# Kernel optimization log

Measured on AMD Instinct MI355X. Metric: run time of the kernel, lower is better.

Reference implementation:

```python
import jax, jax.numpy as jnp
import numpy as np

D_MODEL, N_HEADS, D_FF = 1024, 16, 4096
B, L, PREFIX = 2, 2048, 512
EPS = 1e-5


def _ln(x, w, b):
    mu = jnp.mean(x, axis=-1, keepdims=True)
    var = jnp.mean((x - mu) ** 2, axis=-1, keepdims=True)
    return (x - mu) * jax.lax.rsqrt(var + EPS) * w + b


def setup_inputs() -> dict:
    key = jax.random.key(0)
    ks = jax.random.split(key, 5)
    d, f = D_MODEL, D_FF
    return {
        "x": jax.random.normal(ks[0], (B, L, d), jnp.float32),
        "ln1_w": jnp.ones((d,), jnp.float32),
        "ln1_b": jnp.zeros((d,), jnp.float32),
        "in_proj_w": jax.random.normal(ks[1], (3 * d, d), jnp.float32) / np.sqrt(d),
        "in_proj_b": jnp.zeros((3 * d,), jnp.float32),
        "out_w": jax.random.normal(ks[2], (d, d), jnp.float32) / np.sqrt(d),
        "out_b": jnp.zeros((d,), jnp.float32),
        "ln2_w": jnp.ones((d,), jnp.float32),
        "ln2_b": jnp.zeros((d,), jnp.float32),
        "fc1_w": jax.random.normal(ks[3], (f, d), jnp.float32) / np.sqrt(d),
        "fc1_b": jnp.zeros((f,), jnp.float32),
        "fc2_w": jax.random.normal(ks[4], (d, f), jnp.float32) / np.sqrt(f),
        "fc2_b": jnp.zeros((d,), jnp.float32),
        "prefix_len": PREFIX,
    }


def reference(x, ln1_w, ln1_b, in_proj_w, in_proj_b, out_w, out_b,
              ln2_w, ln2_b, fc1_w, fc1_b, fc2_w, fc2_b, prefix_len):
    Bv, Lv, d = x.shape
    H = N_HEADS
    hd = d // H
    m = prefix_len

    # additive prefix-decoder mask (L, L): allowed if j < m, or (i >= m and j <= i)
    i = jnp.arange(Lv)[:, None]
    j = jnp.arange(Lv)[None, :]
    allowed = (j < m) | ((i >= m) & (j <= i))
    mask = jnp.where(allowed, 0.0, -jnp.inf).astype(x.dtype)

    h = _ln(x, ln1_w, ln1_b)
    qkv = h @ in_proj_w.T + in_proj_b                      # [B, L, 3d]
    q, k, v = jnp.split(qkv, 3, axis=-1)
    q = q.reshape(Bv, Lv, H, hd)
    k = k.reshape(Bv, Lv, H, hd)
    v = v.reshape(Bv, Lv, H, hd)
    scale = 1.0 / np.sqrt(hd)
    scores = jnp.einsum("bihd,bjhd->bhij", q, k) * scale   # [B, H, L, L]
    attn = jax.nn.softmax(scores + mask, axis=-1)
    ctx = jnp.einsum("bhij,bjhd->bihd", attn, v).reshape(Bv, Lv, d)
    sa = ctx @ out_w.T + out_b
    x = x + sa

    h = _ln(x, ln2_w, ln2_b)
    ff = jax.nn.gelu(h @ fc1_w.T + fc1_b, approximate=False) @ fc2_w.T + fc2_b
    return x + ff
```

## Files before the change

kernel.cpp:

```cpp
#include <hip/hip_runtime.h>
#include <cstdint>
#include <cstddef>

#define DM   1024
#define NH   16
#define HD   64
#define DFF  4096
#define BB   2
#define LL   2048
#define MM   (BB*LL)

using short8 = __attribute__((ext_vector_type(8))) short;
using f32x4  = __attribute__((ext_vector_type(4))) float;

__device__ __forceinline__ unsigned short f2bf(float f) {
  union { float f; uint32_t u; } v; v.f = f;
  uint32_t u = v.u;
  uint32_t r = (u + 0x7fffu + ((u >> 16) & 1u)) >> 16;
  return (unsigned short)r;
}

__device__ __forceinline__ uint32_t cvtpk_bf16(float a, float b) {
  uint32_t r;
  asm("v_cvt_pk_bf16_f32 %0, %1, %2" : "=v"(r) : "v"(a), "v"(b));
  return r;
}

__device__ __forceinline__ float exp2_fast(float x) {
  float r;
  asm("v_exp_f32 %0, %1" : "=v"(r) : "v"(x));
  return r;
}

__device__ __forceinline__ float rcp_fast(float x) {
  float r;
  asm("v_rcp_f32 %0, %1" : "=v"(r) : "v"(x));
  return r;
}

__device__ __forceinline__ float gelu_tanh(float v) {
  float y = v * (0.7978845608028654f + 0.035677408136300125f * v * v);
  float e = exp2_fast(y * 2.885390081777927f);
  float tnh = 1.0f - 2.0f * rcp_fast(1.0f + e);
  return 0.5f * v * (1.0f + tnh);
}

#define GLDS16(gp, lp) \
  __builtin_amdgcn_global_load_lds((const __attribute__((address_space(1))) uint32_t*)(gp), \
                                   (__attribute__((address_space(3))) uint32_t*)(lp), 16, 0, 0)

__global__ __launch_bounds__(256) void convert_f32_bf16(const float* __restrict__ in,
                                                        unsigned short* __restrict__ out, int n4) {
  int i = blockIdx.x * 256 + threadIdx.x;
  if (i < n4) {
    float4 v = ((const float4*)in)[i];
    ushort4 o;
    o.x = f2bf(v.x); o.y = f2bf(v.y); o.z = f2bf(v.z); o.w = f2bf(v.w);
    ((ushort4*)out)[i] = o;
  }
}

__global__ __launch_bounds__(256) void convert4(const float* __restrict__ s0, unsigned short* __restrict__ d0, int n0,
                                                const float* __restrict__ s1, unsigned short* __restrict__ d1, int n1,
                                                const float* __restrict__ s2, unsigned short* __restrict__ d2, int n2,
                                                const float* __restrict__ s3, unsigned short* __restrict__ d3, int n3) {
  const int tid = blockIdx.x * 256 + threadIdx.x;
  const int stride = gridDim.x * 256;
  for (int i = tid; i < n0; i += stride) {
    float4 v = ((const float4*)s0)[i];
    ushort4 o; o.x = f2bf(v.x); o.y = f2bf(v.y); o.z = f2bf(v.z); o.w = f2bf(v.w);
    ((ushort4*)d0)[i] = o;
  }
  for (int i = tid; i < n1; i += stride) {
    float4 v = ((const float4*)s1)[i];
    ushort4 o; o.x = f2bf(v.x); o.y = f2bf(v.y); o.z = f2bf(v.z); o.w = f2bf(v.w);
    ((ushort4*)d1)[i] = o;
  }
  for (int i = tid; i < n2; i += stride) {
    float4 v = ((const float4*)s2)[i];
    ushort4 o; o.x = f2bf(v.x); o.y = f2bf(v.y); o.z = f2bf(v.z); o.w = f2bf(v.w);
    ((ushort4*)d2)[i] = o;
  }
  for (int i = tid; i < n3; i += stride) {
    float4 v = ((const float4*)s3)[i];
    ushort4 o; o.x = f2bf(v.x); o.y = f2bf(v.y); o.z = f2bf(v.z); o.w = f2bf(v.w);
    ((ushort4*)d3)[i] = o;
  }
}

__global__ __launch_bounds__(256) void ln_kernel(const float* __restrict__ x,
                                                 const float* __restrict__ w,
                                                 const float* __restrict__ b,
                                                 unsigned short* __restrict__ out) {
  int row = blockIdx.x, t = threadIdx.x;
  float4 v = ((const float4*)(x + (size_t)row * DM))[t];
  float s  = v.x + v.y + v.z + v.w;
  float sq = v.x*v.x + v.y*v.y + v.z*v.z + v.w*v.w;
  #pragma unroll
  for (int o = 32; o; o >>= 1) { s += __shfl_down(s, o); sq += __shfl_down(sq, o); }
  __shared__ float sh[8];
  if ((t & 63) == 0) { sh[t >> 6] = s; sh[4 + (t >> 6)] = sq; }
  __syncthreads();
  float S  = sh[0] + sh[1] + sh[2] + sh[3];
  float SQ = sh[4] + sh[5] + sh[6] + sh[7];
  float mu  = S * (1.0f / DM);
  float var = SQ * (1.0f / DM) - mu * mu;
  float rs  = rsqrtf(var + 1e-5f);
  float4 wv = ((const float4*)w)[t];
  float4 bv = ((const float4*)b)[t];
  ushort4 o;
  o.x = f2bf((v.x - mu) * rs * wv.x + bv.x);
  o.y = f2bf((v.y - mu) * rs * wv.y + bv.y);
  o.z = f2bf((v.z - mu) * rs * wv.z + bv.z);
  o.w = f2bf((v.w - mu) * rs * wv.w + bv.w);
  ((ushort4*)(out + (size_t)row * DM))[t] = o;
}

template <int EPI>
__global__ __launch_bounds__(512) void gemm8(const unsigned short* __restrict__ A,
                                             const unsigned short* __restrict__ Bw,
                                             const float* __restrict__ bias,
                                             unsigned short* __restrict__ Cout,
                                             int M, int N, int K, int lda, int ldb) {
  __shared__ unsigned short As[2][256 * 64];
  __shared__ unsigned short Bs[2][256 * 64];
  const int t = threadIdx.x;
  const int l = t & 63, lr = l & 15, lg = l >> 4;
  const int wid = t >> 6, wm = wid >> 2, wn = wid & 3;

  int bx = blockIdx.x, by = blockIdx.y;
  {
    const int gx = gridDim.x;
    const int total = gx * gridDim.y;
    if ((total & 7) == 0) {
      int lin = by * gx + bx;
      int lin2 = (lin & 7) * (total >> 3) + (lin >> 3);
      bx = lin2 % gx;
      by = lin2 / gx;
    }
  }
  const int m0 = by * 256, n0 = bx * 256;

  f32x4 acc[8][4];
  #pragma unroll
  for (int mi = 0; mi < 8; ++mi)
    #pragma unroll
    for (int ni = 0; ni < 4; ++ni) acc[mi][ni] = {0.f, 0.f, 0.f, 0.f};

  const int rowt = t >> 3, sw = (t & 7) ^ (rowt & 7);
  const unsigned short* Ag = A  + (size_t)(m0 + rowt) * lda + sw * 8;
  const unsigned short* Bg = Bw + (size_t)(n0 + rowt) * ldb + sw * 8;
  const size_t r64A = (size_t)64 * lda;
  const size_t r64B = (size_t)64 * ldb;

  const int rs = lr & 7;
  const int segA = (lg ^ rs) * 8;
  const int segB = ((lg + 4) ^ rs) * 8;

  const int nt = K >> 6;

  auto stage = [&](int kt, int buf) {
    const int k0 = kt << 6;
    char* Ad = (char*)&As[buf][0] + t * 16;
    char* Bd = (char*)&Bs[buf][0] + t * 16;
    #pragma unroll
    for (int g = 0; g < 4; ++g) GLDS16(Ag + k0 + g * r64A, Ad + g * 8192);
    #pragma unroll
    for (int g = 0; g < 4; ++g) GLDS16(Bg + k0 + g * r64B, Bd + g * 8192);
  };

  auto compute = [&](const unsigned short* __restrict__ Ab,
                     const unsigned short* __restrict__ Bb) {
    short8 bfr[4][2];
    #pragma unroll
    for (int ni = 0; ni < 4; ++ni) {
      const int row = wn * 64 + ni * 16 + lr;
      bfr[ni][0] = *(const short8*)&Bb[row * 64 + segA];
      bfr[ni][1] = *(const short8*)&Bb[row * 64 + segB];
    }
    __builtin_amdgcn_s_setprio(1);
    #pragma unroll
    for (int mp = 0; mp < 4; ++mp) {
      short8 af[2][2];
      #pragma unroll
      for (int q = 0; q < 2; ++q) {
        const int row = wm * 128 + (mp * 2 + q) * 16 + lr;
        af[q][0] = *(const short8*)&Ab[row * 64 + segA];
        af[q][1] = *(const short8*)&Ab[row * 64 + segB];
      }
      #pragma unroll
      for (int q = 0; q < 2; ++q)
        #pragma unroll
        for (int ni = 0; ni < 4; ++ni) {
          acc[mp * 2 + q][ni] = __builtin_amdgcn_mfma_f32_16x16x32_bf16(af[q][0], bfr[ni][0], acc[mp * 2 + q][ni], 0, 0, 0);
          acc[mp * 2 + q][ni] = __builtin_amdgcn_mfma_f32_16x16x32_bf16(af[q][1], bfr[ni][1], acc[mp * 2 + q][ni], 0, 0, 0);
        }
    }
    __builtin_amdgcn_s_setprio(0);
  };

  stage(0, 0);
  __syncthreads();

  for (int kt = 0; kt < nt; kt += 2) {
    if (kt + 1 < nt) stage(kt + 1, 1);
    compute(As[0], Bs[0]);
    __syncthreads();
    if (kt + 2 < nt) stage(kt + 2, 0);
    compute(As[1], Bs[1]);
    __syncthreads();
  }

  #pragma unroll
  for (int mi = 0; mi < 8; ++mi) {
    int row = m0 + wm * 128 + mi * 16 + lg * 4;
    #pragma unroll
    for (int ni = 0; ni < 4; ++ni) {
      int col = n0 + wn * 64 + ni * 16 + lr;
      float bv = bias[col];
      #pragma unroll
      for (int r = 0; r < 4; ++r) {
        float v = acc[mi][ni][r] + bv;
        size_t idx = (size_t)(row + r) * N + col;
        if (EPI == 0) {
          Cout[idx] = f2bf(v);
        } else {
          Cout[idx] = f2bf(gelu_tanh(v));
        }
      }
    }
  }
}

template <int EPI, int BM>
__global__ __launch_bounds__(256) void gemm_bt(const unsigned short* __restrict__ A,
                                               const unsigned short* __restrict__ Bw,
                                               const float* __restrict__ bias,
                                               const float* __restrict__ res,
                                               void* __restrict__ Cout,
                                               int M, int N, int K, int lda, int ldb) {
  constexpr int MI   = BM / 32;
  constexpr int ABUF = BM * 64;
  __shared__ unsigned short As[2 * ABUF];
  __shared__ unsigned short Bs[2 * 64 * 64];
  const int t = threadIdx.x;
  const int l = t & 63, lr = l & 15, lg = l >> 4;
  const int w = t >> 6, wm = w >> 1, wn = w & 1;

  int bx = blockIdx.x, by = blockIdx.y;
  {
    const int gx = gridDim.x;
    const int total = gx * gridDim.y;
    if ((total & 7) == 0) {
      int lin = by * gx + bx;
      int lin2 = (lin & 7) * (total >> 3) + (lin >> 3);
      bx = lin2 % gx;
      by = lin2 / gx;
    }
  }
  const int m0 = by * BM, n0 = bx * 64;

  f32x4 acc[MI][2];
  #pragma unroll
  for (int mi = 0; mi < MI; ++mi)
    #pragma unroll
    for (int ni = 0; ni < 2; ++ni) acc[mi][ni] = {0.f, 0.f, 0.f, 0.f};

  const int rowt = t >> 3, sw = (t & 7) ^ (rowt & 7);
  const unsigned short* Ag = A  + (size_t)(m0 + rowt) * lda + sw * 8;
  const unsigned short* Bg = Bw + (size_t)(n0 + rowt) * ldb + sw * 8;
  char* AsB = (char*)As + t * 16;
  char* BsB = (char*)Bs + t * 16;
  const size_t r32A = (size_t)32 * lda;
  const size_t r32B = (size_t)32 * ldb;

  const int rs = lr & 7;
  const int segA = (lg ^ rs) * 8;
  const int segB = ((lg + 4) ^ rs) * 8;

  #pragma unroll
  for (int g = 0; g < MI; ++g) GLDS16(Ag + g * r32A, AsB + g * 4096);
  GLDS16(Bg,        BsB);
  GLDS16(Bg + r32B, BsB + 4096);

  int cur = 0;
  for (int k0 = 0; k0 < K; k0 += 64, cur ^= 1) {
    __syncthreads();
    const int kn = k0 + 64;
    if (kn < K) {
      char* An = AsB + (cur ^ 1) * (ABUF * 2);
      char* Bn = BsB + (cur ^ 1) * 8192;
      #pragma unroll
      for (int g = 0; g < MI; ++g) GLDS16(Ag + kn + g * r32A, An + g * 4096);
      GLDS16(Bg + kn,        Bn);
      GLDS16(Bg + kn + r32B, Bn + 4096);
    }
    const unsigned short* Ab = As + cur * ABUF;
    const unsigned short* Bb = Bs + cur * (64 * 64);
    short8 af[MI][2], bfr[2][2];
    #pragma unroll
    for (int mi = 0; mi < MI; ++mi) {
      const int row = wm * (BM / 2) + mi * 16 + lr;
      af[mi][0] = *(const short8*)&Ab[row * 64 + segA];
      af[mi][1] = *(const short8*)&Ab[row * 64 + segB];
    }
    #pragma unroll
    for (int ni = 0; ni < 2; ++ni) {
      const int row = wn * 32 + ni * 16 + lr;
      bfr[ni][0] = *(const short8*)&Bb[row * 64 + segA];
      bfr[ni][1] = *(const short8*)&Bb[row * 64 + segB];
    }
    #pragma unroll
    for (int mi = 0; mi < MI; ++mi)
      #pragma unroll
      for (int ni = 0; ni < 2; ++ni) {
        acc[mi][ni] = __builtin_amdgcn_mfma_f32_16x16x32_bf16(af[mi][0], bfr[ni][0], acc[mi][ni], 0, 0, 0);
        acc[mi][ni] = __builtin_amdgcn_mfma_f32_16x16x32_bf16(af[mi][1], bfr[ni][1], acc[mi][ni], 0, 0, 0);
      }
  }

  #pragma unroll
  for (int mi = 0; mi < MI; ++mi) {
    int row = m0 + wm * (BM / 2) + mi * 16 + lg * 4;
    #pragma unroll
    for (int ni = 0; ni < 2; ++ni) {
      int col = n0 + wn * 32 + ni * 16 + lr;
      float bv = (EPI == 3) ? 0.f : bias[col];
      #pragma unroll
      for (int r = 0; r < 4; ++r) {
        float v = acc[mi][ni][r] + bv;
        size_t idx = (size_t)(row + r) * N + col;
        if (EPI == 0) {
          ((unsigned short*)Cout)[idx] = f2bf(v);
        } else if (EPI == 1) {
          ((float*)Cout)[idx] = res[idx] + v;
        } else if (EPI == 2) {
          ((unsigned short*)Cout)[idx] = f2bf(gelu_tanh(v));
        } else {
          ((float*)Cout)[idx] += v;
        }
      }
    }
  }
}

__global__ __launch_bounds__(256) void vtrans_kernel(const unsigned short* __restrict__ qkv,
                                                     unsigned short* __restrict__ vt) {
  __shared__ unsigned short tile[64][72];
  int bh = blockIdx.y, b = bh >> 4, h = bh & 15;
  int j0 = blockIdx.x * 64, t = threadIdx.x;
  #pragma unroll
  for (int r = 0; r < 2; ++r) {
    int j = r * 32 + (t >> 3), d0 = (t & 7) * 8;
    short8 v = *(const short8*)(qkv + (size_t)(b * LL + j0 + j) * 3072 + 2048 + h * 64 + d0);
    #pragma unroll
    for (int e = 0; e < 8; ++e) tile[j][d0 + e] = (unsigned short)v[e];
  }
  __syncthreads();
  #pragma unroll
  for (int r = 0; r < 2; ++r) {
    int d = r * 32 + (t >> 3), j = (t & 7) * 8;
    short8 o;
    #pragma unroll
    for (int e = 0; e < 8; ++e) o[e] = (short)tile[j + e][d];
    *(short8*)(vt + (size_t)(bh * 64 + d) * LL + j0 + j) = o;
  }
}

__global__ __launch_bounds__(512) void attn_kernel(const unsigned short* __restrict__ qkv,
                                                   const unsigned short* __restrict__ vt,
                                                   const int* __restrict__ prefix,
                                                   unsigned short* __restrict__ ctx) {
  __shared__ unsigned short Ks[2][64 * 64];
  __shared__ unsigned short Vs[2][64 * 64];
  __shared__ unsigned short Plds[8][16][72];
  const int t = threadIdx.x, w = t >> 6, l = t & 63, lr = l & 15, lg = l >> 4;
  const int bh = blockIdx.y, b = bh >> 4, h = bh & 15;
  const int ib = gridDim.x - 1 - blockIdx.x;
  const int i0 = ib * 128, iw = i0 + w * 16;
  const int m = *prefix;
  const float C = 0.125f * 1.44269504088896f;

  const int r0 = t >> 3, s0 = t & 7, swz = s0 ^ (r0 & 7);
  const unsigned short* Kg0 = qkv + (size_t)(b * LL + r0) * 3072 + DM + h * 64 + swz * 8;
  const unsigned short* Vg0 = vt + (size_t)(bh * 64 + r0) * LL + swz * 8;
  char* KdB = (char*)Ks + t * 16;
  char* VdB = (char*)Vs + t * 16;
  const int rs = lr & 7;
  const int segA = (lg ^ rs) * 8;
  const int segB = ((lg + 4) ^ rs) * 8;

  short8 qf[2];
  {
    const unsigned short* qrow = qkv + (size_t)(b * LL + iw + lr) * 3072 + h * 64;
    qf[0] = *(const short8*)(qrow + lg * 8);
    qf[1] = *(const short8*)(qrow + 32 + lg * 8);
  }
  short8 ones;
  #pragma unroll
  for (int e = 0; e < 8; ++e) ones[e] = (short)0x3F80;

  f32x4 Ot[4];
  #pragma unroll
  for (int dt = 0; dt < 4; ++dt) Ot[dt] = {0.f, 0.f, 0.f, 0.f};
  f32x4 Osum = {0.f, 0.f, 0.f, 0.f};

  const int jmax = (i0 + 128 <= m) ? m : (i0 + 128);
  const int nb = (jmax + 63) >> 6;
  const int i_abs = iw + lr;

  GLDS16(Kg0, KdB);
  GLDS16(Vg0, VdB);

  for (int c = 0; c < nb; ++c) {
    __syncthreads();
    if (c + 1 < nb) {
      const size_t jn = (size_t)(c + 1) * 64;
      const int pn = (c + 1) & 1;
      GLDS16(Kg0 + jn * 3072, KdB + pn * 8192);
      GLDS16(Vg0 + jn,        VdB + pn * 8192);
    }
    const int jt = c * 64, p = c & 1;

    f32x4 sc[4];
    #pragma unroll
    for (int nt = 0; nt < 4; ++nt) {
      sc[nt] = {0.f, 0.f, 0.f, 0.f};
      const int row = nt * 16 + lr;
      short8 kf0 = *(const short8*)&Ks[p][row * 64 + segA];
      short8 kf1 = *(const short8*)&Ks[p][row * 64 + segB];
      sc[nt] = __builtin_amdgcn_mfma_f32_16x16x32_bf16(kf0, qf[0], sc[nt], 0, 0, 0);
      sc[nt] = __builtin_amdgcn_mfma_f32_16x16x32_bf16(kf1, qf[1], sc[nt], 0, 0, 0);
    }
    const bool full = (jt + 64 <= m) || (iw >= m && jt + 64 <= iw + 1);
    #pragma unroll
    for (int nt = 0; nt < 4; ++nt) {
      float p0 = exp2_fast(sc[nt][0] * C);
      float p1 = exp2_fast(sc[nt][1] * C);
      float p2 = exp2_fast(sc[nt][2] * C);
      float p3 = exp2_fast(sc[nt][3] * C);
      if (!full) {
        const int jb = jt + nt * 16 + lg * 4;
        const bool causal_i = (i_abs >= m);
        p0 = ((jb + 0 < m) || (causal_i && jb + 0 <= i_abs)) ? p0 : 0.f;
        p1 = ((jb + 1 < m) || (causal_i && jb + 1 <= i_abs)) ? p1 : 0.f;
        p2 = ((jb + 2 < m) || (causal_i && jb + 2 <= i_abs)) ? p2 : 0.f;
        p3 = ((jb + 3 < m) || (causal_i && jb + 3 <= i_abs)) ? p3 : 0.f;
      }
      uint2 pk;
      pk.x = cvtpk_bf16(p0, p1);
      pk.y = cvtpk_bf16(p2, p3);
      *(uint2*)&Plds[w][lr][nt * 16 + lg * 4] = pk;
    }
    short8 paf0 = *(const short8*)&Plds[w][lr][lg * 8];
    short8 paf1 = *(const short8*)&Plds[w][lr][32 + lg * 8];
    #pragma unroll
    for (int dt = 0; dt < 4; ++dt) {
      const int row = dt * 16 + lr;
      short8 vf0 = *(const short8*)&Vs[p][row * 64 + segA];
      short8 vf1 = *(const short8*)&Vs[p][row * 64 + segB];
      Ot[dt] = __builtin_amdgcn_mfma_f32_16x16x32_bf16(paf0, vf0, Ot[dt], 0, 0, 0);
      Ot[dt] = __builtin_amdgcn_mfma_f32_16x16x32_bf16(paf1, vf1, Ot[dt], 0, 0, 0);
    }
    Osum = __builtin_amdgcn_mfma_f32_16x16x32_bf16(paf0, ones, Osum, 0, 0, 0);
    Osum = __builtin_amdgcn_mfma_f32_16x16x32_bf16(paf1, ones, Osum, 0, 0, 0);
  }
  #pragma unroll
  for (int r = 0; r < 4; ++r) {
    float inv = 1.0f / Osum[r];
    size_t row = (size_t)(b * LL + iw + lg * 4 + r);
    #pragma unroll
    for (int dt = 0; dt < 4; ++dt)
      ctx[row * DM + h * 64 + dt * 16 + lr] = f2bf(Ot[dt][r] * inv);
  }
}

extern "C" void kernel_launch(void* const* d_in, const int* in_sizes, int n_in,
                              void* d_out, int out_size, void* d_ws, size_t ws_size,
                              hipStream_t stream) {
  const float* x        = (const float*)d_in[0];
  const float* ln1_w    = (const float*)d_in[1];
  const float* ln1_b    = (const float*)d_in[2];
  const float* in_proj_w= (const float*)d_in[3];
  const float* in_proj_b= (const float*)d_in[4];
  const float* out_w    = (const float*)d_in[5];
  const float* out_b    = (const float*)d_in[6];
  const float* ln2_w    = (const float*)d_in[7];
  const float* ln2_b    = (const float*)d_in[8];
  const float* fc1_w    = (const float*)d_in[9];
  const float* fc1_b    = (const float*)d_in[10];
  const float* fc2_w    = (const float*)d_in[11];
  const float* fc2_b    = (const float*)d_in[12];
  const int*   prefix   = (const int*)d_in[13];
  float* outp = (float*)d_out;

  char* ws = (char*)d_ws;
  unsigned short* slab  = (unsigned short*)ws;
  float*          x2    = (float*)(ws + ((size_t)8 << 20));
  unsigned short* vtb   = (unsigned short*)(ws + ((size_t)8 << 20));
  unsigned short* wslab = (unsigned short*)(ws + ((size_t)24 << 20));
  unsigned short* qkv   = (unsigned short*)(ws + ((size_t)32 << 20));
  unsigned short* wfc2  = (unsigned short*)(ws + ((size_t)32 << 20));
  unsigned short* ffh   = (unsigned short*)(ws + ((size_t)40 << 20));
  const bool big = ws_size >= ((size_t)72 << 20);
  const bool wd  = ws_size >= ((size_t)80 << 20);

  unsigned short* w_in  = (unsigned short*)(ws + ((size_t)24 << 20));
  unsigned short* w_out = (unsigned short*)(ws + ((size_t)30 << 20));
  unsigned short* w_fc1 = (unsigned short*)(ws + ((size_t)64 << 20));
  unsigned short* w_fc2 = (unsigned short*)(ws + ((size_t)72 << 20));
  unsigned short* ffm32 = (unsigned short*)(ws + ((size_t)32 << 20));

  if (wd) {
    convert4<<<1024, 256, 0, stream>>>(in_proj_w, w_in, 3072 * 1024 / 4,
                                       out_w, w_out, 1024 * 1024 / 4,
                                       fc1_w, w_fc1, 4096 * 1024 / 4,
                                       fc2_w, w_fc2, 1024 * 4096 / 4);
  } else {
    convert_f32_bf16<<<3072, 256, 0, stream>>>(in_proj_w, wslab, 3072 * 1024 / 4);
  }

  ln_kernel<<<MM, 256, 0, stream>>>(x, ln1_w, ln1_b, slab);
  gemm8<0><<<dim3(3072 / 256, MM / 256), 512, 0, stream>>>(slab, wd ? w_in : wslab, in_proj_b, qkv, MM, 3072, 1024, 1024, 1024);
  vtrans_kernel<<<dim3(LL / 64, BB * NH), 256, 0, stream>>>(qkv, vtb);
  attn_kernel<<<dim3(LL / 128, BB * NH), 512, 0, stream>>>(qkv, vtb, prefix, slab);
  if (!wd) convert_f32_bf16<<<1024, 256, 0, stream>>>(out_w, wslab, 1024 * 1024 / 4);
  gemm_bt<1, 64><<<dim3(1024 / 64, MM / 64), 256, 0, stream>>>(slab, wd ? w_out : wslab, out_b, x, x2, MM, 1024, 1024, 1024, 1024);

  ln_kernel<<<MM, 256, 0, stream>>>(x2, ln2_w, ln2_b, slab);
  if (wd) {
    gemm8<2><<<dim3(4096 / 256, MM / 256), 512, 0, stream>>>(slab, w_fc1, fc1_b, ffm32, MM, 4096, 1024, 1024, 1024);
    gemm_bt<1, 64><<<dim3(1024 / 64, MM / 64), 256, 0, stream>>>(ffm32, w_fc2, fc2_b, x2, outp, MM, 1024, 4096, 4096, 4096);
  } else {
    convert_f32_bf16<<<4096, 256, 0, stream>>>(fc1_w, wslab, 4096 * 1024 / 4);
    convert_f32_bf16<<<4096, 256, 0, stream>>>(fc2_w, wfc2, 1024 * 4096 / 4);
    if (big) {
      unsigned short* ffmid = (unsigned short*)(ws + ((size_t)40 << 20));
      gemm8<2><<<dim3(4096 / 256, MM / 256), 512, 0, stream>>>(slab, wslab, fc1_b, ffmid, MM, 4096, 1024, 1024, 1024);
      gemm_bt<1, 64><<<dim3(1024 / 64, MM / 64), 256, 0, stream>>>(ffmid, wfc2, fc2_b, x2, outp, MM, 1024, 4096, 4096, 4096);
    } else {
      gemm_bt<2, 128><<<dim3(2048 / 64, MM / 128), 256, 0, stream>>>(slab, wslab, fc1_b, nullptr, ffh, MM, 2048, 1024, 1024, 1024);
      gemm_bt<1, 64><<<dim3(1024 / 64, MM / 64), 256, 0, stream>>>(ffh, wfc2, fc2_b, x2, outp, MM, 1024, 2048, 2048, 4096);
      gemm_bt<2, 128><<<dim3(2048 / 64, MM / 128), 256, 0, stream>>>(slab, wslab + (size_t)2048 * 1024, fc1_b + 2048, nullptr, ffh, MM, 2048, 1024, 1024, 1024);
      gemm_bt<3, 64><<<dim3(1024 / 64, MM / 64), 256, 0, stream>>>(ffh, wfc2 + 2048, nullptr, nullptr, outp, MM, 1024, 2048, 2048, 4096);
    }
  }
}
```

Before: 223.0 us.

## Fuse LN1 into weight-conversion prep kernel and V-transpose into QKV GEMM epilogue

Merges the first LayerNorm with the bf16 weight conversion into one prep kernel, using extra blocks for the conversion work. The QKV GEMM gains a template flag so blocks covering the V columns write their output directly in transposed per-head layout, removing the separate transpose kernel. This is meant to cut kernel launches and the extra read and write of V. The transposed stores are narrow 8-byte writes strided across rows, which may coalesce poorly.

```diff
diff --git a/kernel.cpp b/kernel.cpp
--- a/kernel.cpp
+++ b/kernel.cpp
@@ -49,50 +49,11 @@
   __builtin_amdgcn_global_load_lds((const __attribute__((address_space(1))) uint32_t*)(gp), \
                                    (__attribute__((address_space(3))) uint32_t*)(lp), 16, 0, 0)
 
-__global__ __launch_bounds__(256) void convert_f32_bf16(const float* __restrict__ in,
-                                                        unsigned short* __restrict__ out, int n4) {
-  int i = blockIdx.x * 256 + threadIdx.x;
-  if (i < n4) {
-    float4 v = ((const float4*)in)[i];
-    ushort4 o;
-    o.x = f2bf(v.x); o.y = f2bf(v.y); o.z = f2bf(v.z); o.w = f2bf(v.w);
-    ((ushort4*)out)[i] = o;
-  }
-}
-
-__global__ __launch_bounds__(256) void convert4(const float* __restrict__ s0, unsigned short* __restrict__ d0, int n0,
-                                                const float* __restrict__ s1, unsigned short* __restrict__ d1, int n1,
-                                                const float* __restrict__ s2, unsigned short* __restrict__ d2, int n2,
-                                                const float* __restrict__ s3, unsigned short* __restrict__ d3, int n3) {
-  const int tid = blockIdx.x * 256 + threadIdx.x;
-  const int stride = gridDim.x * 256;
-  for (int i = tid; i < n0; i += stride) {
-    float4 v = ((const float4*)s0)[i];
-    ushort4 o; o.x = f2bf(v.x); o.y = f2bf(v.y); o.z = f2bf(v.z); o.w = f2bf(v.w);
-    ((ushort4*)d0)[i] = o;
-  }
-  for (int i = tid; i < n1; i += stride) {
-    float4 v = ((const float4*)s1)[i];
-    ushort4 o; o.x = f2bf(v.x); o.y = f2bf(v.y); o.z = f2bf(v.z); o.w = f2bf(v.w);
-    ((ushort4*)d1)[i] = o;
-  }
-  for (int i = tid; i < n2; i += stride) {
-    float4 v = ((const float4*)s2)[i];
-    ushort4 o; o.x = f2bf(v.x); o.y = f2bf(v.y); o.z = f2bf(v.z); o.w = f2bf(v.w);
-    ((ushort4*)d2)[i] = o;
-  }
-  for (int i = tid; i < n3; i += stride) {
-    float4 v = ((const float4*)s3)[i];
-    ushort4 o; o.x = f2bf(v.x); o.y = f2bf(v.y); o.z = f2bf(v.z); o.w = f2bf(v.w);
-    ((ushort4*)d3)[i] = o;
-  }
-}
-
-__global__ __launch_bounds__(256) void ln_kernel(const float* __restrict__ x,
-                                                 const float* __restrict__ w,
-                                                 const float* __restrict__ b,
-                                                 unsigned short* __restrict__ out) {
-  int row = blockIdx.x, t = threadIdx.x;
+__device__ __forceinline__ void ln_row_body(const float* __restrict__ x,
+                                            const float* __restrict__ w,
+                                            const float* __restrict__ b,
+                                            unsigned short* __restrict__ out,
+                                            int row, int t) {
   float4 v = ((const float4*)(x + (size_t)row * DM))[t];
   float s  = v.x + v.y + v.z + v.w;
   float sq = v.x*v.x + v.y*v.y + v.z*v.z + v.w*v.w;
@@ -116,11 +77,67 @@
   ((ushort4*)(out + (size_t)row * DM))[t] = o;
 }
 
-template <int EPI>
+__global__ __launch_bounds__(256) void convert_f32_bf16(const float* __restrict__ in,
+                                                        unsigned short* __restrict__ out, int n4) {
+  int i = blockIdx.x * 256 + threadIdx.x;
+  if (i < n4) {
+    float4 v = ((const float4*)in)[i];
+    ushort4 o;
+    o.x = f2bf(v.x); o.y = f2bf(v.y); o.z = f2bf(v.z); o.w = f2bf(v.w);
+    ((ushort4*)out)[i] = o;
+  }
+}
+
+__global__ __launch_bounds__(256) void prep_kernel(const float* __restrict__ x,
+                                                   const float* __restrict__ ln1_w,
+                                                   const float* __restrict__ ln1_b,
+                                                   unsigned short* __restrict__ h1,
+                                                   const float* __restrict__ s0, unsigned short* __restrict__ d0, int n0,
+                                                   const float* __restrict__ s1, unsigned short* __restrict__ d1, int n1,
+                                                   const float* __restrict__ s2, unsigned short* __restrict__ d2, int n2,
+                                                   const float* __restrict__ s3, unsigned short* __restrict__ d3, int n3) {
+  if (blockIdx.x < MM) {
+    ln_row_body(x, ln1_w, ln1_b, h1, blockIdx.x, threadIdx.x);
+    return;
+  }
+  const int cb = blockIdx.x - MM;
+  const int tid = cb * 256 + threadIdx.x;
+  const int stride = (gridDim.x - MM) * 256;
+  for (int i = tid; i < n0; i += stride) {
+    float4 v = ((const float4*)s0)[i];
+    ushort4 o; o.x = f2bf(v.x); o.y = f2bf(v.y); o.z = f2bf(v.z); o.w = f2bf(v.w);
+    ((ushort4*)d0)[i] = o;
+  }
+  for (int i = tid; i < n1; i += stride) {
+    float4 v = ((const float4*)s1)[i];
+    ushort4 o; o.x = f2bf(v.x); o.y = f2bf(v.y); o.z = f2bf(v.z); o.w = f2bf(v.w);
+    ((ushort4*)d1)[i] = o;
+  }
+  for (int i = tid; i < n2; i += stride) {
+    float4 v = ((const float4*)s2)[i];
+    ushort4 o; o.x = f2bf(v.x); o.y = f2bf(v.y); o.z = f2bf(v.z); o.w = f2bf(v.w);
+    ((ushort4*)d2)[i] = o;
+  }
+  for (int i = tid; i < n3; i += stride) {
+    float4 v = ((const float4*)s3)[i];
+    ushort4 o; o.x = f2bf(v.x); o.y = f2bf(v.y); o.z = f2bf(v.z); o.w = f2bf(v.w);
+    ((ushort4*)d3)[i] = o;
+  }
+}
+
+__global__ __launch_bounds__(256) void ln_kernel(const float* __restrict__ x,
+                                                 const float* __restrict__ w,
+                                                 const float* __restrict__ b,
+                                                 unsigned short* __restrict__ out) {
+  ln_row_body(x, w, b, out, blockIdx.x, threadIdx.x);
+}
+
+template <int EPI, int VT>
 __global__ __launch_bounds__(512) void gemm8(const unsigned short* __restrict__ A,
                                              const unsigned short* __restrict__ Bw,
                                              const float* __restrict__ bias,
                                              unsigned short* __restrict__ Cout,
+                                             unsigned short* __restrict__ vt,
                                              int M, int N, int K, int lda, int ldb) {
   __shared__ unsigned short As[2][256 * 64];
   __shared__ unsigned short Bs[2][256 * 64];
@@ -209,6 +226,25 @@
     if (kt + 2 < nt) stage(kt + 2, 0);
     compute(As[1], Bs[1]);
     __syncthreads();
+  }
+
+  if (VT && n0 >= 2 * DM) {
+    #pragma unroll
+    for (int mi = 0; mi < 8; ++mi) {
+      int row = m0 + wm * 128 + mi * 16 + lg * 4;
+      int b = row >> 11, j = row & (LL - 1);
+      #pragma unroll
+      for (int ni = 0; ni < 4; ++ni) {
+        int col = n0 + wn * 64 + ni * 16 + lr;
+        int hd_ = col - 2 * DM;
+        float bv = bias[col];
+        uint2 pk;
+        pk.x = cvtpk_bf16(acc[mi][ni][0] + bv, acc[mi][ni][1] + bv);
+        pk.y = cvtpk_bf16(acc[mi][ni][2] + bv, acc[mi][ni][3] + bv);
+        *(uint2*)&vt[(size_t)(b * 1024 + hd_) * LL + j] = pk;
+      }
+    }
+    return;
   }
 
   #pragma unroll
@@ -341,29 +377,6 @@
         }
       }
     }
-  }
-}
-
-__global__ __launch_bounds__(256) void vtrans_kernel(const unsigned short* __restrict__ qkv,
-                                                     unsigned short* __restrict__ vt) {
-  __shared__ unsigned short tile[64][72];
-  int bh = blockIdx.y, b = bh >> 4, h = bh & 15;
-  int j0 = blockIdx.x * 64, t = threadIdx.x;
-  #pragma unroll
-  for (int r = 0; r < 2; ++r) {
-    int j = r * 32 + (t >> 3), d0 = (t & 7) * 8;
-    short8 v = *(const short8*)(qkv + (size_t)(b * LL + j0 + j) * 3072 + 2048 + h * 64 + d0);
-    #pragma unroll
-    for (int e = 0; e < 8; ++e) tile[j][d0 + e] = (unsigned short)v[e];
-  }
-  __syncthreads();
-  #pragma unroll
-  for (int r = 0; r < 2; ++r) {
-    int d = r * 32 + (t >> 3), j = (t & 7) * 8;
-    short8 o;
-    #pragma unroll
-    for (int e = 0; e < 8; ++e) o[e] = (short)tile[j + e][d];
-    *(short8*)(vt + (size_t)(bh * 64 + d) * LL + j0 + j) = o;
   }
 }
 
@@ -512,31 +525,31 @@
   unsigned short* ffm32 = (unsigned short*)(ws + ((size_t)32 << 20));
 
   if (wd) {
-    convert4<<<1024, 256, 0, stream>>>(in_proj_w, w_in, 3072 * 1024 / 4,
-                                       out_w, w_out, 1024 * 1024 / 4,
-                                       fc1_w, w_fc1, 4096 * 1024 / 4,
-                                       fc2_w, w_fc2, 1024 * 4096 / 4);
+    prep_kernel<<<MM + 1024, 256, 0, stream>>>(x, ln1_w, ln1_b, slab,
+                                               in_proj_w, w_in, 3072 * 1024 / 4,
+                                               out_w, w_out, 1024 * 1024 / 4,
+                                               fc1_w, w_fc1, 4096 * 1024 / 4,
+                                               fc2_w, w_fc2, 1024 * 4096 / 4);
   } else {
     convert_f32_bf16<<<3072, 256, 0, stream>>>(in_proj_w, wslab, 3072 * 1024 / 4);
-  }
-
-  ln_kernel<<<MM, 256, 0, stream>>>(x, ln1_w, ln1_b, slab);
-  gemm8<0><<<dim3(3072 / 256, MM / 256), 512, 0, stream>>>(slab, wd ? w_in : wslab, in_proj_b, qkv, MM, 3072, 1024, 1024, 1024);
-  vtrans_kernel<<<dim3(LL / 64, BB * NH), 256, 0, stream>>>(qkv, vtb);
+    ln_kernel<<<MM, 256, 0, stream>>>(x, ln1_w, ln1_b, slab);
+  }
+
+  gemm8<0, 1><<<dim3(3072 / 256, MM / 256), 512, 0, stream>>>(slab, wd ? w_in : wslab, in_proj_b, qkv, vtb, MM, 3072, 1024, 1024, 1024);
   attn_kernel<<<dim3(LL / 128, BB * NH), 512, 0, stream>>>(qkv, vtb, prefix, slab);
   if (!wd) convert_f32_bf16<<<1024, 256, 0, stream>>>(out_w, wslab, 1024 * 1024 / 4);
   gemm_bt<1, 64><<<dim3(1024 / 64, MM / 64), 256, 0, stream>>>(slab, wd ? w_out : wslab, out_b, x, x2, MM, 1024, 1024, 1024, 1024);
 
   ln_kernel<<<MM, 256, 0, stream>>>(x2, ln2_w, ln2_b, slab);
   if (wd) {
-    gemm8<2><<<dim3(4096 / 256, MM / 256), 512, 0, stream>>>(slab, w_fc1, fc1_b, ffm32, MM, 4096, 1024, 1024, 1024);
+    gemm8<2, 0><<<dim3(4096 / 256, MM / 256), 512, 0, stream>>>(slab, w_fc1, fc1_b, ffm32, nullptr, MM, 4096, 1024, 1024, 1024);
     gemm_bt<1, 64><<<dim3(1024 / 64, MM / 64), 256, 0, stream>>>(ffm32, w_fc2, fc2_b, x2, outp, MM, 1024, 4096, 4096, 4096);
   } else {
     convert_f32_bf16<<<4096, 256, 0, stream>>>(fc1_w, wslab, 4096 * 1024 / 4);
     convert_f32_bf16<<<4096, 256, 0, stream>>>(fc2_w, wfc2, 1024 * 4096 / 4);
     if (big) {
       unsigned short* ffmid = (unsigned short*)(ws + ((size_t)40 << 20));
-      gemm8<2><<<dim3(4096 / 256, MM / 256), 512, 0, stream>>>(slab, wslab, fc1_b, ffmid, MM, 4096, 1024, 1024, 1024);
+      gemm8<2, 0><<<dim3(4096 / 256, MM / 256), 512, 0, stream>>>(slab, wslab, fc1_b, ffmid, nullptr, MM, 4096, 1024, 1024, 1024);
       gemm_bt<1, 64><<<dim3(1024 / 64, MM / 64), 256, 0, stream>>>(ffmid, wfc2, fc2_b, x2, outp, MM, 1024, 4096, 4096, 4096);
     } else {
       gemm_bt<2, 128><<<dim3(2048 / 64, MM / 128), 256, 0, stream>>>(slab, wslab, fc1_b, nullptr, ffh, MM, 2048, 1024, 1024, 1024);
```

Measured after the change: 221.7 us (median of 3 runs). About the same (-0.6%).
